# Kernel optimization log

Measured on AMD Instinct MI355X. Metric: run time of the kernel, lower is better.

Reference implementation:

```python
import jax, jax.numpy as jnp
import numpy as np

DIM = 2048
DIM_VISUAL = 1024
HEADS = 16
DIM_HEAD = 64
INNER = HEADS * DIM_HEAD  # 1024
EPS = 1e-5


def setup_inputs() -> dict:
    key = jax.random.key(0)
    ks = jax.random.split(key, 6)
    y = jax.random.normal(ks[0], (4, 2048, DIM), dtype=jnp.float32)
    visual_features = jax.random.normal(ks[1], (4, 8, 64, DIM_VISUAL), dtype=jnp.float32)
    ln_g = jnp.ones((DIM,), dtype=jnp.float32)
    ln_b = jnp.zeros((DIM,), dtype=jnp.float32)
    Wq = jax.random.normal(ks[2], (DIM, INNER), dtype=jnp.float32) * 0.02
    Wkv = jax.random.normal(ks[3], (DIM_VISUAL, 2 * INNER), dtype=jnp.float32) * 0.02
    Wo = jax.random.normal(ks[4], (INNER, DIM), dtype=jnp.float32) * 0.02
    return {"y": y, "visual_features": visual_features, "ln_g": ln_g, "ln_b": ln_b,
            "Wq": Wq, "Wkv": Wkv, "Wo": Wo}


def reference(y, visual_features, ln_g, ln_b, Wq, Wkv, Wo):
    scale = DIM_HEAD ** (-0.5)
    b, t, nq, dv = visual_features.shape
    # LayerNorm over last dim
    mu = jnp.mean(y, axis=-1, keepdims=True)
    var = jnp.mean(jnp.square(y - mu), axis=-1, keepdims=True)
    yn = (y - mu) * jax.lax.rsqrt(var + EPS) * ln_g + ln_b
    q = (yn @ Wq) * scale                      # (b, n, inner)
    vis = visual_features.reshape(b, t * nq, dv)
    kv = vis @ Wkv                             # (b, m, 2*inner)
    k, v = jnp.split(kv, 2, axis=-1)
    # split heads: b n (h d) -> b h n d
    split = lambda x: x.reshape(x.shape[0], x.shape[1], HEADS, DIM_HEAD).transpose(0, 2, 1, 3)
    q, k, v = split(q), split(k), split(v)
    sim = jnp.einsum('bhid,bhjd->bhij', q, k)
    alphas = jax.nn.softmax(sim, axis=-1)      # amax-subtract softmax (stable)
    out = jnp.einsum('bhij,bhjd->bhid', alphas, v)
    out = out.transpose(0, 2, 1, 3).reshape(out.shape[0], out.shape[2], INNER)
    return out @ Wo
```

## Files before the change

### kernel.cpp

```cpp
#include <hip/hip_runtime.h>
#include <stdint.h>

typedef unsigned short u16;
typedef __bf16 bfrag __attribute__((ext_vector_type(8)));
typedef float f32x4 __attribute__((ext_vector_type(4)));
typedef u16 u16x4 __attribute__((ext_vector_type(4)));

__device__ __forceinline__ float bf2f(u16 u) {
  union { unsigned i; float f; } x; x.i = ((unsigned)u) << 16; return x.f;
}
__device__ __forceinline__ u16 f2bf(float f) {
  union { unsigned i; float f; } x; x.f = f;
  unsigned r = x.i + 0x7fffu + ((x.i >> 16) & 1u);
  return (u16)(r >> 16);
}
__device__ __forceinline__ unsigned packbf(float lo, float hi) {
  return (unsigned)f2bf(lo) | ((unsigned)f2bf(hi) << 16);
}

__device__ __forceinline__ f32x4 mfma16(bfrag a, bfrag b, f32x4 c) {
  return __builtin_amdgcn_mfma_f32_16x16x32_bf16(a, b, c, 0, 0, 0);
}

__device__ __forceinline__ void gl_lds16(const u16* g, const u16* l) {
  __builtin_amdgcn_global_load_lds(
      (const __attribute__((address_space(1))) unsigned int*)g,
      (__attribute__((address_space(3))) unsigned int*)l, 16, 0, 0);
}

__device__ __forceinline__ void xcd_swizzle(int& bx, int& by) {
  int gx = gridDim.x, nwg = gx * gridDim.y;
  int flat = by * gx + bx;
  int cpx = nwg >> 3;
  int swz = (flat & 7) * cpx + (flat >> 3);
  bx = swz % gx;
  by = swz / gx;
}

__global__ __launch_bounds__(256) void k_transpose(const float* __restrict__ in,
                                                   u16* __restrict__ out, int R, int C) {
  __shared__ u16 tile[32][33];
  int c0 = blockIdx.x * 32, r0 = blockIdx.y * 32;
  int tx = threadIdx.x, ty = threadIdx.y;
#pragma unroll
  for (int i = 0; i < 4; ++i)
    tile[ty + i * 8][tx] = f2bf(in[(size_t)(r0 + ty + i * 8) * C + c0 + tx]);
  __syncthreads();
#pragma unroll
  for (int i = 0; i < 4; ++i)
    out[(size_t)(c0 + ty + i * 8) * R + r0 + tx] = tile[tx][ty + i * 8];
}

__global__ __launch_bounds__(256) void k_cast(const float* __restrict__ in,
                                              u16* __restrict__ out, int n8) {
  int i = blockIdx.x * 256 + threadIdx.x;
  if (i >= n8) return;
  float4 a = *(const float4*)(in + (size_t)i * 8);
  float4 b = *(const float4*)(in + (size_t)i * 8 + 4);
  uint4 ov; u16* po = (u16*)&ov;
  po[0] = f2bf(a.x); po[1] = f2bf(a.y); po[2] = f2bf(a.z); po[3] = f2bf(a.w);
  po[4] = f2bf(b.x); po[5] = f2bf(b.y); po[6] = f2bf(b.z); po[7] = f2bf(b.w);
  *(uint4*)(out + (size_t)i * 8) = ov;
}

__global__ __launch_bounds__(256) void k_layernorm(const float* __restrict__ y,
                                                   const float* __restrict__ g,
                                                   const float* __restrict__ bb,
                                                   u16* __restrict__ yn) {
  int row = blockIdx.x, t = threadIdx.x;
  const float* yr = y + (size_t)row * 2048 + t * 8;
  float4 v0 = *(const float4*)(yr);
  float4 v1 = *(const float4*)(yr + 4);
  float x[8] = {v0.x, v0.y, v0.z, v0.w, v1.x, v1.y, v1.z, v1.w};
  float s = 0.f, ss = 0.f;
#pragma unroll
  for (int j = 0; j < 8; ++j) { s += x[j]; ss += x[j] * x[j]; }
#pragma unroll
  for (int off = 32; off > 0; off >>= 1) {
    s += __shfl_down(s, off);
    ss += __shfl_down(ss, off);
  }
  __shared__ float rs[4], rq[4];
  int lane = t & 63, wid = t >> 6;
  if (lane == 0) { rs[wid] = s; rq[wid] = ss; }
  __syncthreads();
  float S = rs[0] + rs[1] + rs[2] + rs[3];
  float Q = rq[0] + rq[1] + rq[2] + rq[3];
  float mean = S * (1.f / 2048.f);
  float var = Q * (1.f / 2048.f) - mean * mean;
  float rstd = rsqrtf(var + 1e-5f);
  float4 g0 = *(const float4*)(g + t * 8);
  float4 g1 = *(const float4*)(g + t * 8 + 4);
  float4 b0 = *(const float4*)(bb + t * 8);
  float4 b1 = *(const float4*)(bb + t * 8 + 4);
  float gg[8] = {g0.x, g0.y, g0.z, g0.w, g1.x, g1.y, g1.z, g1.w};
  float bv[8] = {b0.x, b0.y, b0.z, b0.w, b1.x, b1.y, b1.z, b1.w};
  uint4 ov; u16* po = (u16*)&ov;
#pragma unroll
  for (int j = 0; j < 8; ++j)
    po[j] = f2bf((x[j] - mean) * rstd * gg[j] + bv[j]);
  *(uint4*)(yn + (size_t)row * 2048 + t * 8) = ov;
}

__device__ __forceinline__ void gemm_pipe(const u16* __restrict__ A,
                                          const u16* __restrict__ Bt,
                                          int K, int m0, int n0,
                                          int wm, int wn, int lr, int lg,
                                          int wid, int lane,
                                          f32x4 (&acc)[4][4]) {
  __shared__ __align__(16) u16 As[2][128 * 64];
  __shared__ __align__(16) u16 Bs[2][128 * 64];
  int sk = lr & 7;
  int srow[4], scol[4], sbase[4];
#pragma unroll
  for (int j = 0; j < 4; ++j) {
    int s0 = (wid * 4 + j) * 64;
    int s = s0 + lane;
    srow[j] = s >> 3;
    scol[j] = ((s & 7) ^ (srow[j] & 7)) * 8;
    sbase[j] = s0 * 8;
  }
  int nk = K >> 6;
#pragma unroll
  for (int pt = 0; pt < 2; ++pt)
#pragma unroll
    for (int j = 0; j < 4; ++j) {
      gl_lds16(A + (size_t)(m0 + srow[j]) * K + pt * 64 + scol[j], As[pt] + sbase[j]);
      gl_lds16(Bt + (size_t)(n0 + srow[j]) * K + pt * 64 + scol[j], Bs[pt] + sbase[j]);
    }
  for (int tt = 0; tt < nk; ++tt) {
    if (tt + 1 < nk)
      asm volatile("s_waitcnt vmcnt(8)" ::: "memory");
    else
      asm volatile("s_waitcnt vmcnt(0)" ::: "memory");
    __builtin_amdgcn_s_barrier();
    __builtin_amdgcn_sched_barrier(0);
    const u16* as = As[tt & 1];
    const u16* bs = Bs[tt & 1];
#pragma unroll
    for (int kk = 0; kk < 2; ++kk) {
      bfrag a[4], b[4];
#pragma unroll
      for (int i = 0; i < 4; ++i)
        a[i] = *(const bfrag*)(as + (wm * 64 + i * 16 + lr) * 64 + (((kk * 4 + lg) ^ sk) * 8));
#pragma unroll
      for (int j = 0; j < 4; ++j)
        b[j] = *(const bfrag*)(bs + (wn * 64 + j * 16 + lr) * 64 + (((kk * 4 + lg) ^ sk) * 8));
      __builtin_amdgcn_s_setprio(1);
#pragma unroll
      for (int i = 0; i < 4; ++i)
#pragma unroll
        for (int j = 0; j < 4; ++j)
          acc[i][j] = mfma16(a[i], b[j], acc[i][j]);
      __builtin_amdgcn_s_setprio(0);
    }
    asm volatile("s_waitcnt lgkmcnt(0)" ::: "memory");
    __builtin_amdgcn_s_barrier();
    __builtin_amdgcn_sched_barrier(0);
    if (tt + 2 < nk) {
      int k0 = (tt + 2) * 64;
#pragma unroll
      for (int j = 0; j < 4; ++j) {
        gl_lds16(A + (size_t)(m0 + srow[j]) * K + k0 + scol[j], As[tt & 1] + sbase[j]);
        gl_lds16(Bt + (size_t)(n0 + srow[j]) * K + k0 + scol[j], Bs[tt & 1] + sbase[j]);
      }
    }
  }
}

template <bool F32OUT>
__global__ __launch_bounds__(256) void k_gemm_bt(const u16* __restrict__ A,
                                                 const u16* __restrict__ Bt,
                                                 void* __restrict__ Cv,
                                                 int M, int N, int K, float scale) {
  int t = threadIdx.x, lane = t & 63, wid = t >> 6;
  int wm = wid >> 1, wn = wid & 1;
  int bx = blockIdx.x, by = blockIdx.y;
  xcd_swizzle(bx, by);
  int m0 = by * 128, n0 = bx * 128;
  int lr = lane & 15, lg = lane >> 4;
  f32x4 acc[4][4];
#pragma unroll
  for (int i = 0; i < 4; ++i)
#pragma unroll
    for (int j = 0; j < 4; ++j) acc[i][j] = (f32x4){0.f, 0.f, 0.f, 0.f};

  gemm_pipe(A, Bt, K, m0, n0, wm, wn, lr, lg, wid, lane, acc);

#pragma unroll
  for (int i = 0; i < 4; ++i)
#pragma unroll
    for (int j = 0; j < 4; ++j) {
      int r0 = m0 + wm * 64 + i * 16 + lg * 4;
      int c0 = n0 + wn * 64 + j * 16 + lr;
#pragma unroll
      for (int r = 0; r < 4; ++r) {
        float v = scale * acc[i][j][r];
        if (F32OUT)
          ((float*)Cv)[(size_t)(r0 + r) * N + c0] = v;
        else
          ((u16*)Cv)[(size_t)(r0 + r) * N + c0] = f2bf(v);
      }
    }
}

__global__ __launch_bounds__(256) void k_gemm_kv(const u16* __restrict__ A,
                                                 const u16* __restrict__ Bt,
                                                 u16* __restrict__ Kb,
                                                 u16* __restrict__ Vtb) {
  const int K = 1024;
  int t = threadIdx.x, lane = t & 63, wid = t >> 6;
  int wm = wid >> 1, wn = wid & 1;
  int bx = blockIdx.x, by = blockIdx.y;
  xcd_swizzle(bx, by);
  int m0 = by * 128, n0 = bx * 128;
  int lr = lane & 15, lg = lane >> 4;
  f32x4 acc[4][4];
#pragma unroll
  for (int i = 0; i < 4; ++i)
#pragma unroll
    for (int j = 0; j < 4; ++j) acc[i][j] = (f32x4){0.f, 0.f, 0.f, 0.f};

  gemm_pipe(A, Bt, K, m0, n0, wm, wn, lr, lg, wid, lane, acc);

#pragma unroll
  for (int i = 0; i < 4; ++i)
#pragma unroll
    for (int j = 0; j < 4; ++j) {
      int r0 = m0 + wm * 64 + i * 16 + lg * 4;
      int c0 = n0 + wn * 64 + j * 16 + lr;
      if (c0 < 1024) {
#pragma unroll
        for (int r = 0; r < 4; ++r)
          Kb[(size_t)(r0 + r) * 1024 + c0] = f2bf(acc[i][j][r]);
      } else {
        int d = c0 - 1024;
        int hh = d >> 6, dd = d & 63;
        int bq = r0 >> 9, kvp = r0 & 511;
        u16x4 pk;
#pragma unroll
        for (int r = 0; r < 4; ++r) pk[r] = f2bf(acc[i][j][r]);
        *(u16x4*)(Vtb + ((size_t)(bq * 16 + hh) * 64 + dd) * 512 + kvp) = pk;
      }
    }
}

__global__ __launch_bounds__(256, 2) void k_attn(const u16* __restrict__ q,
                                                 const u16* __restrict__ kb,
                                                 const u16* __restrict__ vt,
                                                 u16* __restrict__ ao) {
  __shared__ __align__(16) u16 Ks[2][128 * 64];
  __shared__ __align__(16) u16 Vt[2][64 * 128];
  int t = threadIdx.x, lane = t & 63, wid = t >> 6;
  int lr = lane & 15, lg = lane >> 4;
  int sk = lr & 7;
  int a_ = lg >> 1, b_ = lg & 1;
  int bh = blockIdx.y, b = bh >> 4, h = bh & 15;
  int q0 = blockIdx.x * 128 + wid * 32;

  const u16* qg = q + (size_t)(b * 2048 + q0) * 1024 + h * 64;
  bfrag qf[2][2];
#pragma unroll
  for (int rt = 0; rt < 2; ++rt)
#pragma unroll
    for (int kk = 0; kk < 2; ++kk)
      qf[rt][kk] = *(const bfrag*)(qg + (size_t)(rt * 16 + lr) * 1024 + kk * 32 + lg * 8);

  f32x4 o[2][4];
#pragma unroll
  for (int rt = 0; rt < 2; ++rt)
#pragma unroll
    for (int dt = 0; dt < 4; ++dt) o[rt][dt] = (f32x4){0.f, 0.f, 0.f, 0.f};
  float m_s[2] = {-1e30f, -1e30f}, l_s[2] = {0.f, 0.f};

  const u16* kgb = kb + (size_t)(b * 512) * 1024 + h * 64;
  const u16* vgb = vt + (size_t)bh * 64 * 512;

  int krow[4], kcol[4], kbase[4];
#pragma unroll
  for (int j = 0; j < 4; ++j) {
    int g = wid * 4 + j;
    int s = g * 64 + lane;
    krow[j] = s >> 3;
    kcol[j] = ((s & 7) ^ (krow[j] & 7)) * 8;
    kbase[j] = g * 512;
  }

#pragma unroll
  for (int j = 0; j < 4; ++j)
    gl_lds16(kgb + (size_t)krow[j] * 1024 + kcol[j], Ks[0] + kbase[j]);
#pragma unroll
  for (int j = 0; j < 4; ++j) {
    int g = wid * 4 + j;
    int d = g * 4 + (lane >> 4);
    int p = lane & 15;
    gl_lds16(vgb + (size_t)d * 512 + ((p ^ (d & 7)) * 8), Vt[0] + g * 512);
  }
  __syncthreads();

  for (int it = 0; it < 4; ++it) {
    int cur = it & 1;
    if (it + 1 < 4) {
      int kv1 = (it + 1) * 128;
#pragma unroll
      for (int j = 0; j < 4; ++j)
        gl_lds16(kgb + (size_t)(kv1 + krow[j]) * 1024 + kcol[j], Ks[cur ^ 1] + kbase[j]);
#pragma unroll
      for (int j = 0; j < 4; ++j) {
        int g = wid * 4 + j;
        int d = g * 4 + (lane >> 4);
        int p = lane & 15;
        gl_lds16(vgb + (size_t)d * 512 + kv1 + ((p ^ (d & 7)) * 8), Vt[cur ^ 1] + g * 512);
      }
    }
    const u16* ks = Ks[cur];
    const u16* vtl = Vt[cur];

    f32x4 s[2][8];
#pragma unroll
    for (int rt = 0; rt < 2; ++rt)
#pragma unroll
      for (int ct = 0; ct < 8; ++ct) s[rt][ct] = (f32x4){0.f, 0.f, 0.f, 0.f};
    __builtin_amdgcn_s_setprio(1);
#pragma unroll
    for (int ct = 0; ct < 8; ++ct)
#pragma unroll
      for (int kk = 0; kk < 2; ++kk) {
        bfrag kf = *(const bfrag*)(ks + (ct * 16 + lr) * 64 + (((kk * 4 + lg) ^ sk) * 8));
        s[0][ct] = mfma16(kf, qf[0][kk], s[0][ct]);
        s[1][ct] = mfma16(kf, qf[1][kk], s[1][ct]);
      }
    __builtin_amdgcn_s_setprio(0);

    bfrag pf[2][4];
#pragma unroll
    for (int rt = 0; rt < 2; ++rt) {
      float mloc = -1e30f;
#pragma unroll
      for (int ct = 0; ct < 8; ++ct)
#pragma unroll
        for (int r = 0; r < 4; ++r) mloc = fmaxf(mloc, s[rt][ct][r]);
      mloc = fmaxf(mloc, __shfl_xor(mloc, 16));
      mloc = fmaxf(mloc, __shfl_xor(mloc, 32));
      float mn = fmaxf(m_s[rt], mloc);
      float scq = __expf(m_s[rt] - mn);
      float ps = 0.f;
#pragma unroll
      for (int ct = 0; ct < 8; ++ct)
#pragma unroll
        for (int r = 0; r < 4; ++r) {
          float p = __expf(s[rt][ct][r] - mn);
          s[rt][ct][r] = p;
          ps += p;
        }
      ps += __shfl_xor(ps, 16);
      ps += __shfl_xor(ps, 32);
      l_s[rt] = l_s[rt] * scq + ps;
      m_s[rt] = mn;
      float sc4[4];
#pragma unroll
      for (int r = 0; r < 4; ++r) sc4[r] = __shfl(scq, (lane & 48) | (lg * 4 + r));
#pragma unroll
      for (int dt = 0; dt < 4; ++dt)
#pragma unroll
        for (int r = 0; r < 4; ++r) o[rt][dt][r] *= sc4[r];

      unsigned w0[8], w1[8];
#pragma unroll
      for (int ct = 0; ct < 8; ++ct) {
        w0[ct] = packbf(s[rt][ct][0], s[rt][ct][1]);
        w1[ct] = packbf(s[rt][ct][2], s[rt][ct][3]);
      }
#pragma unroll
      for (int kt = 0; kt < 4; ++kt) {
        unsigned c0w0 = w0[2 * kt], c0w1 = w1[2 * kt];
        unsigned c1w0 = w0[2 * kt + 1], c1w1 = w1[2 * kt + 1];
        unsigned s0 = a_ ? c0w0 : c1w0;
        unsigned s1 = a_ ? c0w1 : c1w1;
        unsigned k0 = a_ ? c1w0 : c0w0;
        unsigned k1 = a_ ? c1w1 : c0w1;
        unsigned r0 = (unsigned)__shfl_xor((int)s0, 32);
        unsigned r1 = (unsigned)__shfl_xor((int)s1, 32);
        unsigned x0 = (a_ == b_) ? r0 : k0;
        unsigned x1 = (a_ == b_) ? r1 : k1;
        unsigned kk0 = (a_ == b_) ? k0 : r0;
        unsigned kk1 = (a_ == b_) ? k1 : r1;
        unsigned q0_ = (unsigned)__shfl_xor((int)x0, 16);
        unsigned q1_ = (unsigned)__shfl_xor((int)x1, 16);
        union { unsigned u[4]; bfrag f; } uf;
        uf.u[0] = b_ ? q0_ : kk0;
        uf.u[1] = b_ ? q1_ : kk1;
        uf.u[2] = b_ ? kk0 : q0_;
        uf.u[3] = b_ ? kk1 : q1_;
        pf[rt][kt] = uf.f;
      }
    }

    __builtin_amdgcn_s_setprio(1);
#pragma unroll
    for (int dt = 0; dt < 4; ++dt)
#pragma unroll
      for (int kt = 0; kt < 4; ++kt) {
        int d = dt * 16 + lr;
        bfrag vfb = *(const bfrag*)(vtl + d * 128 + (((kt * 4 + lg) ^ (d & 7)) * 8));
        o[0][dt] = mfma16(pf[0][kt], vfb, o[0][dt]);
        o[1][dt] = mfma16(pf[1][kt], vfb, o[1][dt]);
      }
    __builtin_amdgcn_s_setprio(0);

    if (it + 1 < 4) __syncthreads();
  }

#pragma unroll
  for (int rt = 0; rt < 2; ++rt) {
    float invq = 1.f / l_s[rt];
    float i4[4];
#pragma unroll
    for (int r = 0; r < 4; ++r) i4[r] = __shfl(invq, (lane & 48) | (lg * 4 + r));
#pragma unroll
    for (int dt = 0; dt < 4; ++dt)
#pragma unroll
      for (int r = 0; r < 4; ++r)
        ao[(size_t)(b * 2048 + q0 + rt * 16 + lg * 4 + r) * 1024 + h * 64 + dt * 16 + lr] =
            f2bf(o[rt][dt][r] * i4[r]);
  }
}

extern "C" void kernel_launch(void* const* d_in, const int* in_sizes, int n_in,
                              void* d_out, int out_size, void* d_ws, size_t ws_size,
                              hipStream_t stream) {
  const float* y   = (const float*)d_in[0];
  const float* vf  = (const float*)d_in[1];
  const float* g   = (const float*)d_in[2];
  const float* bb  = (const float*)d_in[3];
  const float* Wq  = (const float*)d_in[4];
  const float* Wkv = (const float*)d_in[5];
  const float* Wo  = (const float*)d_in[6];
  float* out = (float*)d_out;
  char* ws = (char*)d_ws;

  u16* qb   = (u16*)(ws + 0ull);
  u16* kbuf = (u16*)(ws + 16777216ull);
  u16* vtb  = (u16*)(ws + 20971520ull);
  u16* aob  = (u16*)(ws + 25165824ull);
  u16* wqT  = (u16*)(ws + 41943040ull);
  u16* wkvT = (u16*)(ws + 46137344ull);
  u16* woT  = (u16*)(ws + 50331648ull);
  u16* vfb  = (u16*)(ws + 54525952ull);
  u16* yn = (u16*)d_out;

  dim3 tb(32, 8, 1);
  k_transpose<<<dim3(1024 / 32, 2048 / 32, 1), tb, 0, stream>>>(Wq, wqT, 2048, 1024);
  k_transpose<<<dim3(2048 / 32, 1024 / 32, 1), tb, 0, stream>>>(Wkv, wkvT, 1024, 2048);
  k_transpose<<<dim3(2048 / 32, 1024 / 32, 1), tb, 0, stream>>>(Wo, woT, 1024, 2048);
  k_cast<<<(2048 * 1024 / 8 + 255) / 256, 256, 0, stream>>>(vf, vfb, 2048 * 1024 / 8);
  k_layernorm<<<8192, 256, 0, stream>>>(y, g, bb, yn);
  k_gemm_bt<false><<<dim3(1024 / 128, 8192 / 128, 1), 256, 0, stream>>>(yn, wqT, qb, 8192, 1024, 2048, 0.125f);
  k_gemm_kv<<<dim3(2048 / 128, 2048 / 128, 1), 256, 0, stream>>>(vfb, wkvT, kbuf, vtb);
  k_attn<<<dim3(16, 64, 1), 256, 0, stream>>>(qb, kbuf, vtb, aob);
  k_gemm_bt<true><<<dim3(2048 / 128, 8192 / 128, 1), 256, 0, stream>>>(aob, woT, out, 8192, 2048, 1024, 1.0f);
}
```

Baseline: 174.6 us.

## Use 256x256-tile 8-wave GEMM with interleaved prefetch for output projection

Replaces the 128x128 generic GEMM for the output projection (8192x2048x1024) with a dedicated kernel that uses 256x256 tiles, 512 threads and double-buffered LDS. Global-to-LDS prefetches for the next K step are split into chunks and interleaved between MFMA phases, with partial waitcnts and s_setprio to raise MFMA priority. The larger tile reduces global and LDS traffic per FLOP. In exchange it launches only 256 blocks, which may limit occupancy, and uses 64 KB of LDS plus a large register accumulator.

```diff
diff --git a/kernel.cpp b/kernel.cpp
--- a/kernel.cpp
+++ b/kernel.cpp
@@ -242,6 +242,102 @@
         for (int r = 0; r < 4; ++r) pk[r] = f2bf(acc[i][j][r]);
         *(u16x4*)(Vtb + ((size_t)(bq * 16 + hh) * 64 + dd) * 512 + kvp) = pk;
       }
+    }
+}
+
+#define PHASEQ(Q)                                                                      \
+  {                                                                                    \
+    int ra = wm * 128 + (Q) * 32 + lr;                                                 \
+    _Pragma("unroll")                                                                  \
+    for (int kk = 0; kk < 2; ++kk) {                                                   \
+      bfrag a0 = *(const bfrag*)(asl + ra * 64 + (((kk * 4 + lg) ^ sk) * 8));          \
+      bfrag a1 = *(const bfrag*)(asl + (ra + 16) * 64 + (((kk * 4 + lg) ^ sk) * 8));   \
+      __builtin_amdgcn_s_setprio(1);                                                   \
+      _Pragma("unroll")                                                                \
+      for (int j = 0; j < 4; ++j) {                                                    \
+        acc[2 * (Q)][j] = mfma16(a0, bfr[j][kk], acc[2 * (Q)][j]);                     \
+        acc[2 * (Q) + 1][j] = mfma16(a1, bfr[j][kk], acc[2 * (Q) + 1][j]);             \
+      }                                                                                \
+      __builtin_amdgcn_s_setprio(0);                                                   \
+    }                                                                                  \
+  }
+
+__global__ __launch_bounds__(512) void k_gemm_o8(const u16* __restrict__ A,
+                                                 const u16* __restrict__ Bt,
+                                                 float* __restrict__ C) {
+  const int K = 1024, N = 2048;
+  __shared__ __align__(16) u16 As[2][256 * 64];
+  __shared__ __align__(16) u16 Bs[2][256 * 64];
+  int t = threadIdx.x, lane = t & 63, wid = t >> 6;
+  int wm = wid >> 2, wn = wid & 3;
+  int bx = blockIdx.x, by = blockIdx.y;
+  xcd_swizzle(bx, by);
+  int m0 = by * 256, n0 = bx * 256;
+  int lr = lane & 15, lg = lane >> 4;
+  int sk = lr & 7;
+
+  int srow = wid * 8 + (lane >> 3);
+  int scol = ((lane & 7) ^ (srow & 7)) * 8;
+
+  f32x4 acc[8][4];
+#pragma unroll
+  for (int i = 0; i < 8; ++i)
+#pragma unroll
+    for (int j = 0; j < 4; ++j) acc[i][j] = (f32x4){0.f, 0.f, 0.f, 0.f};
+
+  auto stA = [&](int slot, int k0, int c) {
+    gl_lds16(A + (size_t)(m0 + c * 64 + srow) * K + k0 + scol,
+             As[slot] + (c * 64 + wid * 8) * 64);
+  };
+  auto stB = [&](int slot, int k0, int c) {
+    gl_lds16(Bt + (size_t)(n0 + c * 64 + srow) * K + k0 + scol,
+             Bs[slot] + (c * 64 + wid * 8) * 64);
+  };
+
+  const int nk = K >> 6;
+  stB(0, 0, 0); stB(0, 0, 1); stB(0, 0, 2); stB(0, 0, 3);
+  stA(0, 0, 0); stA(0, 0, 2); stA(0, 0, 1); stA(0, 0, 3);
+
+  for (int tt = 0; tt < nk; ++tt) {
+    int sl = tt & 1;
+    int k0n = (tt + 1) << 6;
+    bool pf = (tt + 1 < nk);
+    const u16* asl = As[sl];
+    const u16* bsl = Bs[sl];
+    bfrag bfr[4][2];
+    asm volatile("s_waitcnt vmcnt(2)" ::: "memory");
+    __builtin_amdgcn_s_barrier();
+    __builtin_amdgcn_sched_barrier(0);
+    if (pf) { stB(sl ^ 1, k0n, 0); stB(sl ^ 1, k0n, 1); }
+#pragma unroll
+    for (int j = 0; j < 4; ++j)
+#pragma unroll
+      for (int kk = 0; kk < 2; ++kk)
+        bfr[j][kk] = *(const bfrag*)(bsl + (wn * 64 + j * 16 + lr) * 64 + (((kk * 4 + lg) ^ sk) * 8));
+    PHASEQ(0)
+    if (pf) { stB(sl ^ 1, k0n, 2); stB(sl ^ 1, k0n, 3); }
+    PHASEQ(1)
+    if (pf)
+      asm volatile("s_waitcnt vmcnt(4)" ::: "memory");
+    else
+      asm volatile("s_waitcnt vmcnt(0)" ::: "memory");
+    __builtin_amdgcn_s_barrier();
+    __builtin_amdgcn_sched_barrier(0);
+    if (pf) { stA(sl ^ 1, k0n, 0); stA(sl ^ 1, k0n, 2); }
+    PHASEQ(2)
+    if (pf) { stA(sl ^ 1, k0n, 1); stA(sl ^ 1, k0n, 3); }
+    PHASEQ(3)
+  }
+
+#pragma unroll
+  for (int rt = 0; rt < 8; ++rt)
+#pragma unroll
+    for (int j = 0; j < 4; ++j) {
+      int r0 = m0 + wm * 128 + rt * 16 + lg * 4;
+      int c0 = n0 + wn * 64 + j * 16 + lr;
+#pragma unroll
+      for (int r = 0; r < 4; ++r)
+        C[(size_t)(r0 + r) * N + c0] = acc[rt][j][r];
     }
 }
 
@@ -458,5 +554,5 @@
   k_gemm_bt<false><<<dim3(1024 / 128, 8192 / 128, 1), 256, 0, stream>>>(yn, wqT, qb, 8192, 1024, 2048, 0.125f);
   k_gemm_kv<<<dim3(2048 / 128, 2048 / 128, 1), 256, 0, stream>>>(vfb, wkvT, kbuf, vtb);
   k_attn<<<dim3(16, 64, 1), 256, 0, stream>>>(qb, kbuf, vtb, aob);
-  k_gemm_bt<true><<<dim3(2048 / 128, 8192 / 128, 1), 256, 0, stream>>>(aob, woT, out, 8192, 2048, 1024, 1.0f);
-}
+  k_gemm_o8<<<dim3(2048 / 256, 8192 / 256, 1), 512, 0, stream>>>(aob, woT, out);
+}
```

After: 175.3 us. About the same (+0.4%).

## Replace Q and output GEMMs with 8-wave 256-row tiled pipelined kernel

Applied to the files above, without the earlier changes.

Adds a 512-thread GEMM kernel with 256-row tiles (256x128 for the Q projection, 256x256 for the output projection) whose K loop is split into 32-wide half-steps. Each half-step interleaves LDS fragment loads, next-tile global-to-LDS prefetch and MFMA groups, separated by barriers. The larger tiles raise operand reuse per block and the interleaving is meant to overlap memory traffic with compute. In exchange it uses more LDS and registers per block, adds more barriers per step, and launches fewer blocks, so occupancy and wave balance may suffer.

```diff
diff --git a/kernel.cpp b/kernel.cpp
--- a/kernel.cpp
+++ b/kernel.cpp
@@ -102,6 +102,148 @@
   *(uint4*)(yn + (size_t)row * 2048 + t * 8) = ov;
 }
 
+#define STA(P, KH, K0)                                                          \
+  _Pragma("unroll")                                                             \
+  for (int j = 0; j < 2; ++j)                                                   \
+    gl_lds16(A + (size_t)(m0 + ar[j]) * K + (K0) + (KH) * 32 + ac[j],           \
+             &Ah[P][KH][(wid * 32 + j * 16) * 32]);
+#define STB(P, KH, K0)                                                          \
+  _Pragma("unroll")                                                             \
+  for (int j = 0; j < BC; ++j)                                                  \
+    gl_lds16(Bt + (size_t)(n0 + br[j]) * K + (K0) + (KH) * 32 + bc[j],          \
+             &Bh[P][KH][(wid * BROWS + j * 16) * 32]);
+#define LOADB(P, KH)                                                            \
+  _Pragma("unroll")                                                             \
+  for (int cj = 0; cj < 4; ++cj) {                                              \
+    int rw = wn * 64 + cj * 16 + lr;                                            \
+    bf[cj] = *(const bfrag*)(&Bh[P][KH][rw * 32 + ((lg ^ ((rw >> 1) & 3)) * 8)]); \
+  }
+#define LOADA(P, KH, QP)                                                        \
+  _Pragma("unroll")                                                             \
+  for (int i = 0; i < FRP; ++i) {                                               \
+    int rw = wm * WROWS + ((QP) * FRP + i) * 16 + lr;                           \
+    af[i] = *(const bfrag*)(&Ah[P][KH][rw * 32 + ((lg ^ ((rw >> 1) & 3)) * 8)]); \
+  }
+#define DOMFMA(QP)                                                              \
+  __builtin_amdgcn_s_setprio(1);                                                \
+  _Pragma("unroll")                                                             \
+  for (int i = 0; i < FRP; ++i)                                                 \
+    _Pragma("unroll")                                                           \
+    for (int cj = 0; cj < 4; ++cj)                                              \
+      acc[(QP) * FRP + i][cj] = mfma16(af[i], bf[cj], acc[(QP) * FRP + i][cj]); \
+  __builtin_amdgcn_s_setprio(0);
+#define WAITV()                                                                 \
+  if constexpr (WAIT == 4) asm volatile("s_waitcnt vmcnt(4)" ::: "memory");     \
+  else                     asm volatile("s_waitcnt vmcnt(3)" ::: "memory");
+
+template <int BN, bool F32OUT>
+__global__ __launch_bounds__(512) void k_gemm_8p(const u16* __restrict__ A,
+                                                 const u16* __restrict__ Bt,
+                                                 void* __restrict__ Cv,
+                                                 int N, int K, float scale) {
+  constexpr int WM = (BN == 256) ? 2 : 4;
+  constexpr int WN = 8 / WM;
+  constexpr int WROWS = 256 / WM;
+  constexpr int FR = WROWS / 16;
+  constexpr int FRP = FR / 2;
+  constexpr int BROWS = BN / 8;
+  constexpr int BC = BROWS / 16;
+  constexpr int WAIT = 2 + BC;
+
+  __shared__ __align__(16) u16 Ah[2][2][256 * 32];
+  __shared__ __align__(16) u16 Bh[2][2][BN * 32];
+
+  int t = threadIdx.x, lane = t & 63, wid = t >> 6;
+  int wm = wid / WN, wn = wid % WN;
+  int bx = blockIdx.x, by = blockIdx.y;
+  xcd_swizzle(bx, by);
+  int m0 = by * 256, n0 = bx * BN;
+  int lr = lane & 15, lg = lane >> 4;
+
+  f32x4 acc[FR][4];
+#pragma unroll
+  for (int i = 0; i < FR; ++i)
+#pragma unroll
+    for (int j = 0; j < 4; ++j) acc[i][j] = (f32x4){0.f, 0.f, 0.f, 0.f};
+
+  int ar[2], ac[2];
+#pragma unroll
+  for (int j = 0; j < 2; ++j) {
+    ar[j] = wid * 32 + j * 16 + (lane >> 2);
+    ac[j] = ((lane & 3) ^ ((ar[j] >> 1) & 3)) * 8;
+  }
+  int br[BC], bc[BC];
+#pragma unroll
+  for (int j = 0; j < BC; ++j) {
+    br[j] = wid * BROWS + j * 16 + (lane >> 2);
+    bc[j] = ((lane & 3) ^ ((br[j] >> 1) & 3)) * 8;
+  }
+
+  STA(0, 0, 0) STB(0, 0, 0) STA(0, 1, 0) STB(0, 1, 0)
+
+  int nk = K >> 6;
+  bfrag bf[4], af[FRP];
+
+  for (int tt = 0; tt < nk; ++tt) {
+    int p = tt & 1, pn = p ^ 1;
+    int k0n = (tt + 1) << 6;
+    bool pf = (tt + 1 < nk);
+    WAITV()
+    __builtin_amdgcn_s_barrier();
+    __builtin_amdgcn_sched_barrier(0);
+    LOADB(p, 0) LOADA(p, 0, 0)
+    if (pf) { STA(pn, 0, k0n) }
+    __builtin_amdgcn_s_barrier();
+    asm volatile("s_waitcnt lgkmcnt(0)" ::: "memory");
+    __builtin_amdgcn_sched_barrier(0);
+    DOMFMA(0)
+    LOADA(p, 0, 1)
+    if (pf) { STB(pn, 0, k0n) }
+    __builtin_amdgcn_s_barrier();
+    asm volatile("s_waitcnt lgkmcnt(0)" ::: "memory");
+    __builtin_amdgcn_sched_barrier(0);
+    DOMFMA(1)
+    if (pf) { WAITV() }
+    else    { asm volatile("s_waitcnt vmcnt(0)" ::: "memory"); }
+    __builtin_amdgcn_s_barrier();
+    __builtin_amdgcn_sched_barrier(0);
+    LOADB(p, 1) LOADA(p, 1, 0)
+    if (pf) { STA(pn, 1, k0n) }
+    __builtin_amdgcn_s_barrier();
+    asm volatile("s_waitcnt lgkmcnt(0)" ::: "memory");
+    __builtin_amdgcn_sched_barrier(0);
+    DOMFMA(0)
+    LOADA(p, 1, 1)
+    if (pf) { STB(pn, 1, k0n) }
+    __builtin_amdgcn_s_barrier();
+    asm volatile("s_waitcnt lgkmcnt(0)" ::: "memory");
+    __builtin_amdgcn_sched_barrier(0);
+    DOMFMA(1)
+  }
+
+#pragma unroll
+  for (int fr = 0; fr < FR; ++fr)
+#pragma unroll
+    for (int cj = 0; cj < 4; ++cj) {
+      int r0 = m0 + wm * WROWS + fr * 16 + lg * 4;
+      int c0 = n0 + wn * 64 + cj * 16 + lr;
+#pragma unroll
+      for (int r = 0; r < 4; ++r) {
+        float v = scale * acc[fr][cj][r];
+        if (F32OUT)
+          ((float*)Cv)[(size_t)(r0 + r) * N + c0] = v;
+        else
+          ((u16*)Cv)[(size_t)(r0 + r) * N + c0] = f2bf(v);
+      }
+    }
+}
+#undef STA
+#undef STB
+#undef LOADB
+#undef LOADA
+#undef DOMFMA
+#undef WAITV
+
 __device__ __forceinline__ void gemm_pipe(const u16* __restrict__ A,
                                           const u16* __restrict__ Bt,
                                           int K, int m0, int n0,
@@ -166,42 +308,6 @@
       }
     }
   }
-}
-
-template <bool F32OUT>
-__global__ __launch_bounds__(256) void k_gemm_bt(const u16* __restrict__ A,
-                                                 const u16* __restrict__ Bt,
-                                                 void* __restrict__ Cv,
-                                                 int M, int N, int K, float scale) {
-  int t = threadIdx.x, lane = t & 63, wid = t >> 6;
-  int wm = wid >> 1, wn = wid & 1;
-  int bx = blockIdx.x, by = blockIdx.y;
-  xcd_swizzle(bx, by);
-  int m0 = by * 128, n0 = bx * 128;
-  int lr = lane & 15, lg = lane >> 4;
-  f32x4 acc[4][4];
-#pragma unroll
-  for (int i = 0; i < 4; ++i)
-#pragma unroll
-    for (int j = 0; j < 4; ++j) acc[i][j] = (f32x4){0.f, 0.f, 0.f, 0.f};
-
-  gemm_pipe(A, Bt, K, m0, n0, wm, wn, lr, lg, wid, lane, acc);
-
-#pragma unroll
-  for (int i = 0; i < 4; ++i)
-#pragma unroll
-    for (int j = 0; j < 4; ++j) {
-      int r0 = m0 + wm * 64 + i * 16 + lg * 4;
-      int c0 = n0 + wn * 64 + j * 16 + lr;
-#pragma unroll
-      for (int r = 0; r < 4; ++r) {
-        float v = scale * acc[i][j][r];
-        if (F32OUT)
-          ((float*)Cv)[(size_t)(r0 + r) * N + c0] = v;
-        else
-          ((u16*)Cv)[(size_t)(r0 + r) * N + c0] = f2bf(v);
-      }
-    }
 }
 
 __global__ __launch_bounds__(256) void k_gemm_kv(const u16* __restrict__ A,
@@ -455,8 +561,8 @@
   k_transpose<<<dim3(2048 / 32, 1024 / 32, 1), tb, 0, stream>>>(Wo, woT, 1024, 2048);
   k_cast<<<(2048 * 1024 / 8 + 255) / 256, 256, 0, stream>>>(vf, vfb, 2048 * 1024 / 8);
   k_layernorm<<<8192, 256, 0, stream>>>(y, g, bb, yn);
-  k_gemm_bt<false><<<dim3(1024 / 128, 8192 / 128, 1), 256, 0, stream>>>(yn, wqT, qb, 8192, 1024, 2048, 0.125f);
+  k_gemm_8p<128, false><<<dim3(1024 / 128, 8192 / 256, 1), 512, 0, stream>>>(yn, wqT, qb, 1024, 2048, 0.125f);
   k_gemm_kv<<<dim3(2048 / 128, 2048 / 128, 1), 256, 0, stream>>>(vfb, wkvT, kbuf, vtb);
   k_attn<<<dim3(16, 64, 1), 256, 0, stream>>>(qb, kbuf, vtb, aob);
-  k_gemm_bt<true><<<dim3(2048 / 128, 8192 / 128, 1), 256, 0, stream>>>(aob, woT, out, 8192, 2048, 1024, 1.0f);
-}
+  k_gemm_8p<256, true><<<dim3(2048 / 256, 8192 / 256, 1), 512, 0, stream>>>(aob, woT, out, 2048, 1024, 1.0f);
+}
```

Result: slower. 180.4 us (+3.3%).
